# Kernel tuning notes

Measured on AMD Instinct MI355X. Metric: run time of the kernel, lower is better.

Reference implementation:

```python
import jax, jax.numpy as jnp
import numpy as np

H = 16       # query heads
KV = 4       # key/value heads
HD = 256     # head dim
ROPE_THETA = 10000.0
EPS = 1e-6


def _rms_norm(x, w):
    # Gemma RMSNorm over last dim: x / rms * (1 + w), computed in fp32
    xf = x.astype(jnp.float32)
    var = jnp.mean(xf * xf, axis=-1, keepdims=True)
    out = xf * jax.lax.rsqrt(var + EPS) * (1.0 + w.astype(jnp.float32))
    return out.astype(x.dtype)


def _rope_cos_sin(position_ids):
    # cos/sin tables of shape [S, HD]
    inv_freq = 1.0 / (ROPE_THETA ** (jnp.arange(0, HD, 2, dtype=jnp.float32) / HD))
    ang = position_ids.astype(jnp.float32)[:, None] * inv_freq[None, :]  # [S, HD/2]
    emb = jnp.concatenate([ang, ang], axis=-1)                           # [S, HD]
    return jnp.cos(emb), jnp.sin(emb)


def _rotate_half(x):
    x1, x2 = jnp.split(x, 2, axis=-1)
    return jnp.concatenate([-x2, x1], axis=-1)


def _apply_rope(x, cos, sin):
    # x: [B, h, S, HD]; cos/sin: [S, HD] -> broadcast over batch and heads
    c = cos[None, None, :, :]
    s = sin[None, None, :, :]
    return (x * c + _rotate_half(x) * s).astype(x.dtype)


def setup_inputs() -> dict:
    key = jax.random.key(0)
    ks = jax.random.split(key, 8)
    B, S, D = 2, 2048, 2048
    inp = {
        "hidden_states": jax.random.normal(ks[0], (B, S, D), jnp.float32),
        "Wq": jax.random.normal(ks[1], (D, H * HD), jnp.float32) * 0.02,
        "Wk": jax.random.normal(ks[2], (D, KV * HD), jnp.float32) * 0.02,
        "Wv": jax.random.normal(ks[3], (D, KV * HD), jnp.float32) * 0.02,
        "Wo": jax.random.normal(ks[4], (H * HD, D), jnp.float32) * 0.02,
        "q_norm_w": jnp.zeros((HD,), jnp.float32),
        "k_norm_w": jnp.zeros((HD,), jnp.float32),
        "position_ids": jnp.arange(S, dtype=jnp.int32),
    }
    return inp


def reference(hidden_states, Wq, Wk, Wv, Wo, q_norm_w, k_norm_w, position_ids):
    B, S, D = hidden_states.shape
    scale = HD ** -0.5

    # projections -> [B, h, S, HD]
    q = jnp.einsum("bsd,de->bse", hidden_states, Wq).reshape(B, S, H, HD).transpose(0, 2, 1, 3)
    k = jnp.einsum("bsd,de->bse", hidden_states, Wk).reshape(B, S, KV, HD).transpose(0, 2, 1, 3)
    v = jnp.einsum("bsd,de->bse", hidden_states, Wv).reshape(B, S, KV, HD).transpose(0, 2, 1, 3)

    # Gemma per-head RMSNorm on q/k
    q = _rms_norm(q, q_norm_w)
    k = _rms_norm(k, k_norm_w)

    # RoPE
    cos, sin = _rope_cos_sin(position_ids)
    q = _apply_rope(q, cos, sin)
    k = _apply_rope(k, cos, sin)

    # GQA: repeat kv heads to match query heads
    rep = H // KV
    k = jnp.repeat(k, rep, axis=1)  # [B, H, S, HD]
    v = jnp.repeat(v, rep, axis=1)

    # SDPA with causal mask, softmax in fp32
    scores = jnp.einsum("bhqd,bhkd->bhqk", q, k) * scale
    causal = jnp.tril(jnp.ones((S, S), dtype=bool))
    scores = jnp.where(causal[None, None, :, :], scores, jnp.finfo(jnp.float32).min)
    probs = jax.nn.softmax(scores.astype(jnp.float32), axis=-1).astype(q.dtype)
    attn = jnp.einsum("bhqk,bhkd->bhqd", probs, v)  # [B, H, S, HD]

    attn = attn.transpose(0, 2, 1, 3).reshape(B, S, H * HD)
    return jnp.einsum("bse,ed->bsd", attn, Wo)
```

## Files before the change

### kernel.cpp

```cpp
#include <hip/hip_runtime.h>

typedef unsigned short ushort_t;
typedef __bf16 bf16_t;
typedef bf16_t bf16x8 __attribute__((ext_vector_type(8)));
typedef float floatx4 __attribute__((ext_vector_type(4)));
typedef ushort_t ushort4v __attribute__((ext_vector_type(4)));
typedef ushort_t ushort8v __attribute__((ext_vector_type(8)));

static constexpr int B = 2, S = 2048, D = 2048;
static constexpr int H = 16, KVH = 4, HD = 256;

#define DEVFN static __device__ __forceinline__

DEVFN ushort_t f2b(float f) {
  union { float f; unsigned u; } x; x.f = f;
  unsigned r = x.u + 0x7fffu + ((x.u >> 16) & 1u);
  return (ushort_t)(r >> 16);
}
DEVFN float b2f(ushort_t h) {
  union { unsigned u; float f; } x; x.u = ((unsigned)h) << 16;
  return x.f;
}
DEVFN void gll16(const void* g, void* l) {
  __builtin_amdgcn_global_load_lds(
      (const __attribute__((address_space(1))) void*)g,
      (__attribute__((address_space(3))) void*)l, 16, 0, 0);
}

DEVFN void bar() {
  asm volatile("" ::: "memory");
  __builtin_amdgcn_s_barrier();
  asm volatile("" ::: "memory");
}
template <int N>
DEVFN void waitvm() { asm volatile("s_waitcnt vmcnt(%0)" ::"n"(N) : "memory"); }

DEVFN ushort4v norm_rope_row(ushort4v raw, const float* __restrict__ w,
                             const float* __restrict__ tab, int s, float scale, int lane) {
  float v[4];
  float ss = 0.f;
#pragma unroll
  for (int i = 0; i < 4; i++) { v[i] = b2f(raw[i]); ss += v[i] * v[i]; }
#pragma unroll
  for (int m = 1; m < 64; m <<= 1) ss += __shfl_xor(ss, m, 64);
  const float inv = rsqrtf(ss * (1.0f / HD) + 1e-6f);
  float4 wv = *(const float4*)(w + lane * 4);
  float y[4];
  y[0] = v[0] * inv * (1.0f + wv.x);
  y[1] = v[1] * inv * (1.0f + wv.y);
  y[2] = v[2] * inv * (1.0f + wv.z);
  y[3] = v[3] * inv * (1.0f + wv.w);
  float py[4];
#pragma unroll
  for (int i = 0; i < 4; i++) py[i] = __shfl_xor(y[i], 32, 64);
  const bool lo = (lane < 32);
  ushort4v ov;
#pragma unroll
  for (int i = 0; i < 4; i++) {
    int dd = (lane * 4 + i) & 127;
    float2 cs = *(const float2*)(tab + ((size_t)s * 128 + dd) * 2);
    float rot = lo ? -py[i] : py[i];
    ov[i] = f2b((y[i] * cs.x + rot * cs.y) * scale);
  }
  return ov;
}

__global__ void k_cvt_bf16(const float* __restrict__ in, ushort_t* __restrict__ out, int n) {
  int i = (blockIdx.x * 256 + threadIdx.x) * 4;
  if (i >= n) return;
  float4 v = *(const float4*)(in + i);
  ushort4v o;
  o[0] = f2b(v.x); o[1] = f2b(v.y); o[2] = f2b(v.z); o[3] = f2b(v.w);
  *(ushort4v*)(out + i) = o;
}

__global__ void k_transpose_cvt(const float* __restrict__ in, ushort_t* __restrict__ out,
                                int R, int C) {
  __shared__ float tile[64][65];
  const int cb = blockIdx.x * 64, rb = blockIdx.y * 64;
  const int t = threadIdx.x;
  const int l16 = t & 15, g16 = t >> 4;
#pragma unroll
  for (int p = 0; p < 4; p++) {
    const int r = p * 16 + g16;
    float4 v = *(const float4*)(in + (size_t)(rb + r) * C + cb + l16 * 4);
    tile[r][l16 * 4 + 0] = v.x;
    tile[r][l16 * 4 + 1] = v.y;
    tile[r][l16 * 4 + 2] = v.z;
    tile[r][l16 * 4 + 3] = v.w;
  }
  __syncthreads();
#pragma unroll
  for (int p = 0; p < 4; p++) {
    const int c = p * 16 + g16;
    ushort4v o4;
#pragma unroll
    for (int i = 0; i < 4; i++) o4[i] = f2b(tile[l16 * 4 + i][c]);
    *(ushort4v*)(out + (size_t)(cb + c) * R + rb + l16 * 4) = o4;
  }
}

__global__ void k_rope_table(const int* __restrict__ pos_ids, float* __restrict__ tab) {
  int idx = blockIdx.x * 256 + threadIdx.x;
  int s = idx >> 7, dd = idx & 127;
  float ang = (float)pos_ids[s] * exp2f((float)dd * (-13.287712379549449f / 128.0f));
  tab[idx * 2] = cosf(ang);
  tab[idx * 2 + 1] = sinf(ang);
}

DEVFN void stage_tile(const ushort_t* __restrict__ A, const ushort_t* __restrict__ Bt,
                      ushort_t* smb, size_t arow0, size_t brow0, int K, int kt) {
  const int t = threadIdx.x;
  const int rq = t >> 2;
  const int cq = (t & 3) * 8;
#pragma unroll
  for (int i = 0; i < 2; i++) {
    const int cs = cq ^ ((rq & 8) << 1);
    gll16(A + (arow0 + rq) * (size_t)K + kt + i * 32 + cs, smb + i * 4096 + t * 8);
  }
#pragma unroll
  for (int i = 0; i < 4; i++) {
    const int row = ((i & 1) << 7) | rq;
    const int cs = cq ^ ((row & 8) << 1);
    gll16(Bt + (brow0 + row) * (size_t)K + kt + (i >> 1) * 32 + cs,
          smb + 8192 + i * 4096 + t * 8);
  }
}

DEVFN bf16x8 ldsA(const ushort_t* buf, int row, int ks, int lq) {
  const int c = (lq * 8) ^ ((row & 8) << 1);
  return *(const bf16x8*)(buf + ks * 4096 + row * 32 + c);
}
DEVFN bf16x8 ldsB(const ushort_t* buf, int row, int ks, int lq) {
  const int c = (lq * 8) ^ ((row & 8) << 1);
  return *(const bf16x8*)(buf + 8192 + ks * 8192 + row * 32 + c);
}

template <int MODE>
__global__ __launch_bounds__(512, 2)
void k_gemm256(const ushort_t* __restrict__ A, const ushort_t* __restrict__ Bt,
               void* __restrict__ C0, void* __restrict__ C1, void* __restrict__ C2,
               int N, int K) {
  __shared__ ushort_t sm[49152];
  const int tid = threadIdx.x;
  const int lane = tid & 63, wave = tid >> 6;
  const int lr = lane & 15, lq = lane >> 4;
  const int wm = wave >> 2, wn = wave & 3;
  const size_t m0 = (size_t)blockIdx.x * 128;
  const size_t n0 = (size_t)blockIdx.y * 256;

  floatx4 acc[4][4];
#pragma unroll
  for (int i = 0; i < 4; i++)
#pragma unroll
    for (int j = 0; j < 4; j++) acc[i][j] = {0.f, 0.f, 0.f, 0.f};

  const int NT = K >> 6;
  stage_tile(A, Bt, sm, m0, n0, K, 0);
  stage_tile(A, Bt, sm + 24576, m0, n0, K, 64);

  for (int t = 0; t < NT; ++t) {
    ushort_t* bA = sm + (t & 1) * 24576;
    if (t < NT - 1) waitvm<6>(); else waitvm<0>();
    bar();

    bf16x8 a[2][4], bfr[2][4];
#pragma unroll
    for (int ks = 0; ks < 2; ks++) {
#pragma unroll
      for (int m = 0; m < 4; m++) a[ks][m] = ldsA(bA, wm * 64 + m * 16 + lr, ks, lq);
#pragma unroll
      for (int n = 0; n < 4; n++) bfr[ks][n] = ldsB(bA, wn * 64 + n * 16 + lr, ks, lq);
    }
    __builtin_amdgcn_s_setprio(1);
#pragma unroll
    for (int m = 0; m < 4; m++)
#pragma unroll
      for (int n = 0; n < 4; n++)
        acc[m][n] = __builtin_amdgcn_mfma_f32_16x16x32_bf16(a[0][m], bfr[0][n], acc[m][n], 0, 0, 0);
    __builtin_amdgcn_s_setprio(0);
    asm volatile("s_waitcnt lgkmcnt(0)" ::: "memory");
    __builtin_amdgcn_sched_barrier(0);
    bar();
    if (t + 2 < NT) stage_tile(A, Bt, bA, m0, n0, K, (t + 2) * 64);
    __builtin_amdgcn_sched_barrier(0);
    __builtin_amdgcn_s_setprio(1);
#pragma unroll
    for (int m = 0; m < 4; m++)
#pragma unroll
      for (int n = 0; n < 4; n++)
        acc[m][n] = __builtin_amdgcn_mfma_f32_16x16x32_bf16(a[1][m], bfr[1][n], acc[m][n], 0, 0, 0);
    __builtin_amdgcn_s_setprio(0);
  }

  const int colb = (int)n0;
#pragma unroll
  for (int mg = 0; mg < 4; mg++)
#pragma unroll
    for (int ng = 0; ng < 4; ng++) {
      const size_t row0 = m0 + wm * 64 + mg * 16 + lq * 4;
      const int col = colb + wn * 64 + ng * 16 + lr;
      if (MODE == 1) {
#pragma unroll
        for (int r = 0; r < 4; r++)
          ((float*)C0)[(row0 + r) * N + col] = acc[mg][ng][r];
      } else {
        if (colb < 4096) {
#pragma unroll
        for (int r = 0; r < 4; r++)
            ((ushort_t*)C0)[(row0 + r) * 4096 + col] = f2b(acc[mg][ng][r]);
        } else if (colb < 5120) {
#pragma unroll
          for (int r = 0; r < 4; r++)
            ((ushort_t*)C1)[(row0 + r) * 1024 + (col - 4096)] = f2b(acc[mg][ng][r]);
        } else {
          const int ch = col - 5120;
          const int kvh = ch >> 8, chh = ch & 255, f = chh >> 4, lrv = chh & 15;
          const size_t bb = row0 >> 11;
          const int s0 = (int)(row0 & 2047);
          const int tile = s0 >> 6, kh = (s0 >> 5) & 1, lqv = (s0 >> 3) & 3, j0 = s0 & 7;
          ushort4v pk;
#pragma unroll
          for (int r = 0; r < 4; r++) pk[r] = f2b(acc[mg][ng][r]);
          *(ushort4v*)&((ushort_t*)C2)[((bb * KVH + kvh) * (S / 64) + tile) * 16384 +
                                       (size_t)(f * 2 + kh) * 512 +
                                       (size_t)(lqv * 16 + lrv) * 8 + j0] = pk;
        }
      }
    }
}

__global__ void k_norm_rope_k(const ushort_t* __restrict__ Kb, ushort_t* __restrict__ Kf,
                              const float* __restrict__ w, const float* __restrict__ tab) {
  __shared__ ushort_t t[64 * 264];
  const int lane = threadIdx.x & 63, wave = threadIdx.x >> 6;
  const int tile = blockIdx.x, kvh = blockIdx.y, b = blockIdx.z;
#pragma unroll
  for (int rr = 0; rr < 16; rr++) {
    const int row = wave * 16 + rr;
    const int s = tile * 64 + row;
    const ushort_t* p = Kb + ((size_t)(b * S + s) * KVH + kvh) * HD + lane * 4;
    ushort4v raw = *(const ushort4v*)p;
    *(ushort4v*)&t[row * 264 + lane * 4] = norm_rope_row(raw, w, tab, s, 1.0f, lane);
  }
  __syncthreads();
  ushort_t* dst = Kf + ((size_t)(b * KVH + kvh) * (S / 64) + tile) * 16384;
  const int lr = lane & 15, lq = lane >> 4;
#pragma unroll
  for (int q = 0; q < 8; q++) {
    const int c = wave * 8 + q;
    const int nt = c >> 3, ks = c & 7;
    ushort8v v = *(const ushort8v*)&t[(nt * 16 + lr) * 264 + ks * 32 + lq * 8];
    *(ushort8v*)&dst[(size_t)c * 512 + lane * 8] = v;
  }
}

__global__ __launch_bounds__(256, 2)
void k_attn(const ushort_t* __restrict__ Q, const ushort_t* __restrict__ Kf,
            const ushort_t* __restrict__ Vf, ushort_t* __restrict__ O,
            const float* __restrict__ qw, const float* __restrict__ tab) {
  __shared__ ushort_t Ks[16384];
  __shared__ ushort_t Vs[16384];
  __shared__ ushort_t Ps[4][16 * 72];
  const int lane = threadIdx.x & 63, wave = threadIdx.x >> 6;
  const int lr = lane & 15, lq = lane >> 4;
  const int lin = blockIdx.x;
  const int g = lin & 7, j = lin >> 3;
  const int b = g >> 2, kvh = g & 3;
  const int h = kvh * 4 + (j >> 4);
  const int xq = j & 15;
  const size_t kvb = (size_t)(b * KVH + kvh) * (S / 64);

#pragma unroll 1
  for (int half = 0; half < 2; half++) {
    const int qt = half ? xq : (S / 64 - 1 - xq);
    const int q0 = qt * 64 + wave * 16;
    const int sq = q0 + lr;
    const int ntiles = qt + 1;

    {
      const ushort_t* tb = Kf + kvb * 16384;
      const ushort_t* vb = Vf + kvb * 16384;
#pragma unroll
      for (int i = 0; i < 8; i++) {
        const int c = wave * 8 + i;
        gll16(tb + (size_t)c * 512 + lane * 8, &Ks[c * 512 + lane * 8]);
      }
#pragma unroll
      for (int i = 0; i < 8; i++) {
        const int c = wave * 8 + i;
        gll16(vb + (size_t)c * 512 + lane * 8, &Vs[c * 512 + lane * 8]);
      }
    }

    bf16x8 qf[8];
    {
      const ushort_t* qp = Q + ((size_t)(b * S + sq) * H + h) * HD + lq * 8;
      ushort8v qr[8];
#pragma unroll
      for (int ks = 0; ks < 8; ks++) qr[ks] = *(const ushort8v*)(qp + ks * 32);
      float ss = 0.f;
#pragma unroll
      for (int ks = 0; ks < 8; ks++)
#pragma unroll
        for (int jj = 0; jj < 8; jj++) { float v = b2f(qr[ks][jj]); ss += v * v; }
      ss += __shfl_xor(ss, 16, 64);
      ss += __shfl_xor(ss, 32, 64);
      const float inv = rsqrtf(ss * (1.0f / HD) + 1e-6f);
      const float sc = 0.0625f * 1.4426950408889634f;
#pragma unroll
      for (int c = 0; c < 4; c++) {
        const int d0 = c * 32 + lq * 8;
        float wl[8], wh[8];
        {
          float4 a0 = *(const float4*)(qw + d0);
          float4 a1 = *(const float4*)(qw + d0 + 4);
          float4 a2 = *(const float4*)(qw + d0 + 128);
          float4 a3 = *(const float4*)(qw + d0 + 132);
          wl[0]=a0.x; wl[1]=a0.y; wl[2]=a0.z; wl[3]=a0.w;
          wl[4]=a1.x; wl[5]=a1.y; wl[6]=a1.z; wl[7]=a1.w;
          wh[0]=a2.x; wh[1]=a2.y; wh[2]=a2.z; wh[3]=a2.w;
          wh[4]=a3.x; wh[5]=a3.y; wh[6]=a3.z; wh[7]=a3.w;
        }
        const float* tp = tab + ((size_t)sq * 128 + d0) * 2;
        ushort8v olo, ohi;
#pragma unroll
        for (int jj = 0; jj < 8; jj++) {
          float ylo = b2f(qr[c][jj]) * inv * (1.0f + wl[jj]);
          float yhi = b2f(qr[c + 4][jj]) * inv * (1.0f + wh[jj]);
          float2 cs = *(const float2*)(tp + jj * 2);
          olo[jj] = f2b((ylo * cs.x - yhi * cs.y) * sc);
          ohi[jj] = f2b((yhi * cs.x + ylo * cs.y) * sc);
        }
        qf[c] = *reinterpret_cast<bf16x8*>(&olo);
        qf[c + 4] = *reinterpret_cast<bf16x8*>(&ohi);
      }
    }

    floatx4 o[16];
#pragma unroll
    for (int f = 0; f < 16; f++) o[f] = {0.f, 0.f, 0.f, 0.f};
    float m_i[4] = {-1e30f, -1e30f, -1e30f, -1e30f};
    float l_i[4] = {0.f, 0.f, 0.f, 0.f};

    waitvm<8>();
    bar();

    for (int kt = 0; kt < ntiles; kt++) {
      const int kbase = kt * 64;
      const bool last = (kt == ntiles - 1);

      const int ntmax = min(4, ((q0 + 15 - kbase) >> 4) + 1);
      floatx4 sacc[4];
      __builtin_amdgcn_s_setprio(1);
#pragma unroll
      for (int nt = 0; nt < 4; nt++) {
        if (nt < ntmax) {
          sacc[nt] = {0.f, 0.f, 0.f, 0.f};
#pragma unroll
          for (int ks = 0; ks < 8; ks++) {
            bf16x8 kf = *(const bf16x8*)&Ks[(nt * 8 + ks) * 512 + lane * 8];
            sacc[nt] = __builtin_amdgcn_mfma_f32_16x16x32_bf16(qf[ks], kf, sacc[nt], 0, 0, 0);
          }
        } else {
          sacc[nt] = {-1e30f, -1e30f, -1e30f, -1e30f};
        }
      }
      __builtin_amdgcn_s_setprio(0);

      if (kbase + 63 > q0) {
#pragma unroll
        for (int nt = 0; nt < 4; nt++)
          if (nt < ntmax)
#pragma unroll
            for (int r = 0; r < 4; r++)
              if (kbase + nt * 16 + lr > q0 + lq * 4 + r) sacc[nt][r] = -1e30f;
      }
      float mt[4], alpha[4], rs[4];
#pragma unroll
      for (int r = 0; r < 4; r++)
        mt[r] = fmaxf(fmaxf(sacc[0][r], sacc[1][r]), fmaxf(sacc[2][r], sacc[3][r]));
#pragma unroll
      for (int m = 1; m < 16; m <<= 1)
#pragma unroll
        for (int r = 0; r < 4; r++) mt[r] = fmaxf(mt[r], __shfl_xor(mt[r], m, 64));
#pragma unroll
      for (int r = 0; r < 4; r++) {
        float mn = fmaxf(m_i[r], mt[r]);
        alpha[r] = exp2f(m_i[r] - mn);
        m_i[r] = mn;
      }
#pragma unroll
      for (int nt = 0; nt < 4; nt++)
#pragma unroll
        for (int r = 0; r < 4; r++) sacc[nt][r] = exp2f(sacc[nt][r] - m_i[r]);
#pragma unroll
      for (int r = 0; r < 4; r++)
        rs[r] = (sacc[0][r] + sacc[1][r]) + (sacc[2][r] + sacc[3][r]);
#pragma unroll
      for (int m = 1; m < 16; m <<= 1)
#pragma unroll
        for (int r = 0; r < 4; r++) rs[r] += __shfl_xor(rs[r], m, 64);
#pragma unroll
      for (int r = 0; r < 4; r++) l_i[r] = l_i[r] * alpha[r] + rs[r];
      if (__any((alpha[0] < 1.f) | (alpha[1] < 1.f) | (alpha[2] < 1.f) | (alpha[3] < 1.f))) {
#pragma unroll
        for (int f = 0; f < 16; f++) {
          o[f][0] *= alpha[0]; o[f][1] *= alpha[1];
          o[f][2] *= alpha[2]; o[f][3] *= alpha[3];
        }
      }
      ushort_t* psw = Ps[wave];
#pragma unroll
      for (int nt = 0; nt < 4; nt++)
#pragma unroll
        for (int r = 0; r < 4; r++)
          psw[(lq * 4 + r) * 72 + nt * 16 + lr] = f2b(sacc[nt][r]);
      bf16x8 pf0 = *(const bf16x8*)&psw[lr * 72 + lq * 8];
      bf16x8 pf1 = *(const bf16x8*)&psw[lr * 72 + 32 + lq * 8];

      asm volatile("s_waitcnt lgkmcnt(0)" ::: "memory");
      __builtin_amdgcn_sched_barrier(0);
      waitvm<0>();
      bar();

      if (!last) {
        const ushort_t* tb = Kf + (kvb + kt + 1) * 16384;
#pragma unroll
        for (int i = 0; i < 8; i++) {
          const int c = wave * 8 + i;
          gll16(tb + (size_t)c * 512 + lane * 8, &Ks[c * 512 + lane * 8]);
        }
      }

      __builtin_amdgcn_s_setprio(1);
#pragma unroll
      for (int f = 0; f < 16; f++) {
        bf16x8 vf0 = *(const bf16x8*)&Vs[(f * 2 + 0) * 512 + lane * 8];
        o[f] = __builtin_amdgcn_mfma_f32_16x16x32_bf16(pf0, vf0, o[f], 0, 0, 0);
        bf16x8 vf1 = *(const bf16x8*)&Vs[(f * 2 + 1) * 512 + lane * 8];
        o[f] = __builtin_amdgcn_mfma_f32_16x16x32_bf16(pf1, vf1, o[f], 0, 0, 0);
      }
      __builtin_amdgcn_s_setprio(0);

      asm volatile("s_waitcnt lgkmcnt(0)" ::: "memory");
      __builtin_amdgcn_sched_barrier(0);
      waitvm<0>();
      bar();

      if (!last) {
        const ushort_t* vb = Vf + (kvb + kt + 1) * 16384;
#pragma unroll
        for (int i = 0; i < 8; i++) {
          const int c = wave * 8 + i;
          gll16(vb + (size_t)c * 512 + lane * 8, &Vs[c * 512 + lane * 8]);
        }
      }
    }
    float invl[4];
#pragma unroll
    for (int r = 0; r < 4; r++) invl[r] = 1.0f / l_i[r];
#pragma unroll
    for (int f = 0; f < 16; f++)
#pragma unroll
      for (int r = 0; r < 4; r++)
        O[((size_t)(b * S + q0 + lq * 4 + r) * H + h) * HD + f * 16 + lr] =
            f2b(o[f][r] * invl[r]);
  }
}

extern "C" void kernel_launch(void* const* d_in, const int* in_sizes, int n_in,
                              void* d_out, int out_size, void* d_ws, size_t ws_size,
                              hipStream_t stream) {
  const float* hs = (const float*)d_in[0];
  const float* Wq = (const float*)d_in[1];
  const float* Wk = (const float*)d_in[2];
  const float* Wv = (const float*)d_in[3];
  const float* Wo = (const float*)d_in[4];
  const float* qw = (const float*)d_in[5];
  const float* kw = (const float*)d_in[6];
  const int* pos = (const int*)d_in[7];
  float* out = (float*)d_out;

  char* ws = (char*)d_ws;
  size_t off = 0;
  auto alloc = [&](size_t bytes) {
    void* p = ws + off;
    off += (bytes + 255) & ~(size_t)255;
    return p;
  };
  ushort_t* Xb   = (ushort_t*)alloc((size_t)B * S * D * 2);
  ushort_t* Wqt  = (ushort_t*)alloc((size_t)(H * HD) * D * 2);
  ushort_t* Wkvt = (ushort_t*)alloc((size_t)(2 * KVH * HD) * D * 2);
  ushort_t* Wot  = (ushort_t*)alloc((size_t)D * (H * HD) * 2);
  ushort_t* Qb   = (ushort_t*)alloc((size_t)B * S * H * HD * 2);
  ushort_t* Kf   = (ushort_t*)alloc((size_t)B * S * KVH * HD * 2);
  ushort_t* Vf   = (ushort_t*)alloc((size_t)B * S * KVH * HD * 2);
  ushort_t* Ab   = (ushort_t*)alloc((size_t)B * S * H * HD * 2);
  float*    tab  = (float*)alloc((size_t)S * 128 * 2 * sizeof(float));
  ushort_t* Kb = Ab;

  k_cvt_bf16<<<(B * S * D / 4 + 255) / 256, 256, 0, stream>>>(hs, Xb, B * S * D);
  k_transpose_cvt<<<dim3((H * HD) / 64, D / 64), 256, 0, stream>>>(Wq, Wqt, D, H * HD);
  k_transpose_cvt<<<dim3((KVH * HD) / 64, D / 64), 256, 0, stream>>>(Wk, Wkvt, D, KVH * HD);
  k_transpose_cvt<<<dim3((KVH * HD) / 64, D / 64), 256, 0, stream>>>(
      Wv, Wkvt + (size_t)(KVH * HD) * D, D, KVH * HD);
  k_transpose_cvt<<<dim3(D / 64, (H * HD) / 64), 256, 0, stream>>>(Wo, Wot, H * HD, D);
  k_rope_table<<<S * 128 / 256, 256, 0, stream>>>(pos, tab);

  k_gemm256<0><<<dim3((B * S) / 128, 6144 / 256), 512, 0, stream>>>(
      Xb, Wqt, Qb, Kb, Vf, 6144, D);

  k_norm_rope_k<<<dim3(S / 64, KVH, B), 256, 0, stream>>>(Kb, Kf, kw, tab);

  k_attn<<<512, 256, 0, stream>>>(Qb, Kf, Vf, Ab, qw, tab);

  k_gemm256<1><<<dim3((B * S) / 128, D / 256), 512, 0, stream>>>(
      Ab, Wot, out, nullptr, nullptr, D, H * HD);
}
```

Before: 530.3 us.

## Replace prefetched K/V double-stage pipeline with synchronous per-tile loads in attention

The attention kernel no longer prefetches the next K tile during PV and the next V tile after it. Each key tile now issues both its K and V loads into LDS at the start of the iteration, bracketed by two block barriers. The s_setprio hints around the MFMA sections are removed as well. This simplifies synchronisation and cuts the barrier count from two mid-loop waits to a load-then-wait pattern, but it exposes the global-to-LDS load latency on every tile instead of hiding it behind compute.

```diff
diff --git a/kernel.cpp b/kernel.cpp
--- a/kernel.cpp
+++ b/kernel.cpp
@@ -207,7 +207,7 @@
       } else {
         if (colb < 4096) {
 #pragma unroll
-        for (int r = 0; r < 4; r++)
+          for (int r = 0; r < 4; r++)
             ((ushort_t*)C0)[(row0 + r) * 4096 + col] = f2b(acc[mg][ng][r]);
         } else if (colb < 5120) {
 #pragma unroll
@@ -259,8 +259,8 @@
 void k_attn(const ushort_t* __restrict__ Q, const ushort_t* __restrict__ Kf,
             const ushort_t* __restrict__ Vf, ushort_t* __restrict__ O,
             const float* __restrict__ qw, const float* __restrict__ tab) {
-  __shared__ ushort_t Ks[16384];
-  __shared__ ushort_t Vs[16384];
+  __shared__ ushort_t Ks[32 * 512];
+  __shared__ ushort_t Vs[32 * 512];
   __shared__ ushort_t Ps[4][16 * 72];
   const int lane = threadIdx.x & 63, wave = threadIdx.x >> 6;
   const int lr = lane & 15, lq = lane >> 4;
@@ -276,22 +276,6 @@
     const int qt = half ? xq : (S / 64 - 1 - xq);
     const int q0 = qt * 64 + wave * 16;
     const int sq = q0 + lr;
-    const int ntiles = qt + 1;
-
-    {
-      const ushort_t* tb = Kf + kvb * 16384;
-      const ushort_t* vb = Vf + kvb * 16384;
-#pragma unroll
-      for (int i = 0; i < 8; i++) {
-        const int c = wave * 8 + i;
-        gll16(tb + (size_t)c * 512 + lane * 8, &Ks[c * 512 + lane * 8]);
-      }
-#pragma unroll
-      for (int i = 0; i < 8; i++) {
-        const int c = wave * 8 + i;
-        gll16(vb + (size_t)c * 512 + lane * 8, &Vs[c * 512 + lane * 8]);
-      }
-    }
 
     bf16x8 qf[8];
     {
@@ -343,16 +327,22 @@
     float m_i[4] = {-1e30f, -1e30f, -1e30f, -1e30f};
     float l_i[4] = {0.f, 0.f, 0.f, 0.f};
 
-    waitvm<8>();
-    bar();
-
+    const int ntiles = qt + 1;
     for (int kt = 0; kt < ntiles; kt++) {
       const int kbase = kt * 64;
-      const bool last = (kt == ntiles - 1);
+      __syncthreads();
+      const ushort_t* tb = Kf + (kvb + kt) * 16384;
+      const ushort_t* vb = Vf + (kvb + kt) * 16384;
+#pragma unroll
+      for (int i = 0; i < 16; i++) {
+        const int c = wave * 16 + i;
+        if (c < 32) gll16(tb + (size_t)c * 512 + lane * 8, &Ks[c * 512 + lane * 8]);
+        else        gll16(vb + (size_t)(c - 32) * 512 + lane * 8, &Vs[(c - 32) * 512 + lane * 8]);
+      }
+      __syncthreads();
 
       const int ntmax = min(4, ((q0 + 15 - kbase) >> 4) + 1);
       floatx4 sacc[4];
-      __builtin_amdgcn_s_setprio(1);
 #pragma unroll
       for (int nt = 0; nt < 4; nt++) {
         if (nt < ntmax) {
@@ -366,8 +356,6 @@
           sacc[nt] = {-1e30f, -1e30f, -1e30f, -1e30f};
         }
       }
-      __builtin_amdgcn_s_setprio(0);
-
       if (kbase + 63 > q0) {
 #pragma unroll
         for (int nt = 0; nt < 4; nt++)
@@ -418,43 +406,12 @@
           psw[(lq * 4 + r) * 72 + nt * 16 + lr] = f2b(sacc[nt][r]);
       bf16x8 pf0 = *(const bf16x8*)&psw[lr * 72 + lq * 8];
       bf16x8 pf1 = *(const bf16x8*)&psw[lr * 72 + 32 + lq * 8];
-
-      asm volatile("s_waitcnt lgkmcnt(0)" ::: "memory");
-      __builtin_amdgcn_sched_barrier(0);
-      waitvm<0>();
-      bar();
-
-      if (!last) {
-        const ushort_t* tb = Kf + (kvb + kt + 1) * 16384;
-#pragma unroll
-        for (int i = 0; i < 8; i++) {
-          const int c = wave * 8 + i;
-          gll16(tb + (size_t)c * 512 + lane * 8, &Ks[c * 512 + lane * 8]);
-        }
-      }
-
-      __builtin_amdgcn_s_setprio(1);
 #pragma unroll
       for (int f = 0; f < 16; f++) {
         bf16x8 vf0 = *(const bf16x8*)&Vs[(f * 2 + 0) * 512 + lane * 8];
         o[f] = __builtin_amdgcn_mfma_f32_16x16x32_bf16(pf0, vf0, o[f], 0, 0, 0);
         bf16x8 vf1 = *(const bf16x8*)&Vs[(f * 2 + 1) * 512 + lane * 8];
         o[f] = __builtin_amdgcn_mfma_f32_16x16x32_bf16(pf1, vf1, o[f], 0, 0, 0);
-      }
-      __builtin_amdgcn_s_setprio(0);
-
-      asm volatile("s_waitcnt lgkmcnt(0)" ::: "memory");
-      __builtin_amdgcn_sched_barrier(0);
-      waitvm<0>();
-      bar();
-
-      if (!last) {
-        const ushort_t* vb = Vf + (kvb + kt + 1) * 16384;
-#pragma unroll
-        for (int i = 0; i < 8; i++) {
-          const int c = wave * 8 + i;
-          gll16(vb + (size_t)c * 512 + lane * 8, &Vs[c * 512 + lane * 8]);
-        }
       }
     }
     float invl[4];
```

Measured after the change: 505.1 us. 1.05x faster.
